# Kernel optimization log

Hardware: AMD Instinct MI355X
Metric: run time of the kernel (lower is better)

## Reference

```python
import jax, jax.numpy as jnp
import numpy as np

N = 50000          # nodes
E = 800000         # edges (before self loops)
F_IN = 16
HID = 64
HEADS = 4
C = 64             # per-head out channels (concat=False)
G = 64             # graphs in batch
NEG_SLOPE = 0.2


def setup_inputs() -> dict:
    key = jax.random.key(0)
    ks = jax.random.split(key, 20)
    inp = {
        "x": jax.random.normal(ks[0], (N, F_IN), jnp.float32),
        "edge_index": jax.random.randint(ks[1], (2, E), 0, N, jnp.int64),
        "batch": jnp.sort(jax.random.randint(ks[2], (N,), 0, G, jnp.int64)),
        "W_in": jax.random.normal(ks[3], (HID, F_IN), jnp.float32) * 0.1,
        "b_in": jnp.zeros((HID,), jnp.float32),
        "W_out": jax.random.normal(ks[4], (1, HID), jnp.float32) * 0.1,
        "b_out": jnp.zeros((1,), jnp.float32),
    }
    for l in range(3):
        inp[f"W{l}"] = jax.random.normal(ks[5 + 4 * l], (HEADS * C, HID), jnp.float32) * 0.1
        inp[f"asrc{l}"] = jax.random.normal(ks[6 + 4 * l], (HEADS, C), jnp.float32) * 0.1
        inp[f"adst{l}"] = jax.random.normal(ks[7 + 4 * l], (HEADS, C), jnp.float32) * 0.1
        inp[f"bg{l}"] = jnp.zeros((HID,), jnp.float32)
    return inp


def _gat_layer(x, W, a_src, a_dst, bias, src, dst, n):
    # x: [N, HID] -> h: [N, HEADS, C]
    h = (x @ W.T).reshape(n, HEADS, C)
    alpha_s = jnp.einsum("nhc,hc->nh", h, a_src)   # [N, H]
    alpha_d = jnp.einsum("nhc,hc->nh", h, a_dst)
    e = jax.nn.leaky_relu(alpha_s[src] + alpha_d[dst], NEG_SLOPE)  # [E', H]
    # segment softmax over incoming edges of each dst node
    m = jax.ops.segment_max(e, dst, num_segments=n)
    e = jnp.exp(e - m[dst])
    s = jax.ops.segment_sum(e, dst, num_segments=n)
    alpha = e / (s[dst] + 1e-16)                                   # [E', H]
    msg = alpha[:, :, None] * h[src]                               # [E', H, C]
    out = jax.ops.segment_sum(msg, dst, num_segments=n)            # [N, H, C]
    return out.mean(axis=1) + bias                                 # concat=False: head mean


def reference(x, W_in, b_in, W0, asrc0, adst0, bg0, W1, asrc1, adst1, bg1,
              W2, asrc2, adst2, bg2, W_out, b_out, edge_index, batch):
    n = x.shape[0]
    # add self loops (PyG GATConv default)
    loops = jnp.arange(n, dtype=edge_index.dtype)
    src = jnp.concatenate([edge_index[0], loops])
    dst = jnp.concatenate([edge_index[1], loops])

    h = x @ W_in.T + b_in
    for W, a_s, a_d, bg in ((W0, asrc0, adst0, bg0),
                            (W1, asrc1, adst1, bg1),
                            (W2, asrc2, adst2, bg2)):
        h = jax.nn.relu(_gat_layer(h, W, a_s, a_d, bg, src, dst, n))
        # dropout p=0.2 is inactive in eval mode

    # global mean pool over graphs
    sums = jax.ops.segment_sum(h, batch, num_segments=G)
    cnt = jax.ops.segment_sum(jnp.ones((n,), h.dtype), batch, num_segments=G)
    graph_emb = sums / jnp.maximum(cnt, 1.0)[:, None]              # [G, HID]

    return jax.nn.sigmoid(graph_emb @ W_out.T + b_out)             # [G, 1]
```

## Files before the change

kernel.cpp:

```cpp
#include <hip/hip_runtime.h>
#include <hip/hip_bf16.h>
#include <hip/hip_fp16.h>

#define HID 64
#define HEADS 4
#define GCNT 64
#define F_IN 16
#define NEG 0.2f
#define NBUCK 256
#define BSLOT 6144
#define SCHUNK 2048

typedef _Float16 f16x8 __attribute__((ext_vector_type(8)));
typedef float f32x4 __attribute__((ext_vector_type(4)));

__device__ __forceinline__ unsigned pack_h2(float a, float b) {
  __half2 h = __floats2half2_rn(a, b);
  union { __half2 h; unsigned u; } c;
  c.h = h;
  return c.u;
}
__device__ __forceinline__ __half2 uas_h2(unsigned u) {
  union { unsigned u; __half2 h; } c;
  c.u = u;
  return c.h;
}
__device__ __forceinline__ unsigned h2_as_u(__half2 h) {
  union { __half2 h; unsigned u; } c;
  c.h = h;
  return c.u;
}
__device__ __forceinline__ __half2 xor16_add(__half2 v) {
  unsigned u = (unsigned)__shfl_xor((int)h2_as_u(v), 16, 64);
  return __hadd2(v, uas_h2(u));
}

__global__ __launch_bounds__(256) void k_pre(
    const float* __restrict__ W0, const float* __restrict__ asrc,
    const float* __restrict__ adst, int* __restrict__ bcur, float* __restrict__ va) {
  int t = threadIdx.x;
  if (blockIdx.x == 0) bcur[t] = 0;
  int idx = blockIdx.x * 256 + t;
  int q = idx >> 6, k = idx & 63;
  const float* a = (q < 4) ? asrc : adst;
  int h = q & 3;
  float s = 0.f;
  for (int c = 0; c < 64; ++c) s += a[h * 64 + c] * W0[(h * 64 + c) * 64 + k];
  va[idx] = s;
}

__global__ __launch_bounds__(256) void k_bucket(
    const int* __restrict__ ei, int* __restrict__ bcur,
    unsigned* __restrict__ tmp, int E, int N) {
  __shared__ int hist[NBUCK];
  __shared__ int base[NBUCK];
  int t = threadIdx.x;
  int start = blockIdx.x * SCHUNK;
  int end = min(start + SCHUNK, E + N);
  hist[t] = 0;
  __syncthreads();
  unsigned val[8];
  int rank[8];
  bool ok[8];
#pragma unroll
  for (int k = 0; k < 8; ++k) {
    int i = start + t + k * 256;
    ok[k] = i < end;
    if (ok[k]) {
      int s, d;
      if (i < E) {
        s = ei[i];
        d = ei[E + i];
      } else {
        s = d = i - E;
      }
      val[k] = ((unsigned)d << 16) | (unsigned)s;
      rank[k] = atomicAdd(&hist[d >> 8], 1);
    }
  }
  __syncthreads();
  int h = hist[t];
  base[t] = h ? atomicAdd(&bcur[t], h) : 0;
  __syncthreads();
#pragma unroll
  for (int k = 0; k < 8; ++k) {
    if (ok[k]) {
      int bk = (int)(val[k] >> 24);
      int idx = base[bk] + rank[k];
      if (idx < BSLOT) tmp[(size_t)bk * BSLOT + idx] = val[k];
    }
  }
}

__global__ __launch_bounds__(256) void k_bsort(
    const unsigned* __restrict__ tmp, const int* __restrict__ bcur,
    int* __restrict__ rowptr, int* __restrict__ col, int N) {
  __shared__ int s[NBUCK];
  __shared__ int hist[NBUCK];
  __shared__ int pref[NBUCK];
  int b = blockIdx.x, t = threadIdx.x;
  int c = min(bcur[t], BSLOT);
  s[t] = c;
  __syncthreads();
  for (int o = 1; o < 256; o <<= 1) {
    int x = (t >= o) ? s[t - o] : 0;
    __syncthreads();
    s[t] += x;
    __syncthreads();
  }
  int base = (b == 0) ? 0 : s[b - 1];
  int total = s[255];
  int cntb = min(bcur[b], BSLOT);
  hist[t] = 0;
  __syncthreads();
  for (int j = t; j < cntb; j += 256)
    atomicAdd(&hist[(tmp[(size_t)b * BSLOT + j] >> 16) & 255], 1);
  __syncthreads();
  int v = hist[t];
  pref[t] = v;
  __syncthreads();
  for (int o = 1; o < 256; o <<= 1) {
    int x = (t >= o) ? pref[t - o] : 0;
    __syncthreads();
    pref[t] += x;
    __syncthreads();
  }
  pref[t] -= v;
  __syncthreads();
  int node = b * 256 + t;
  if (node < N) rowptr[node] = base + pref[t];
  if (b == 255 && t == 255) rowptr[N] = total;
  hist[t] = 0;
  __syncthreads();
  for (int j = t; j < cntb; j += 256) {
    unsigned e = tmp[(size_t)b * BSLOT + j];
    int d8 = (int)((e >> 16) & 255);
    int r = atomicAdd(&hist[d8], 1);
    col[base + pref[d8] + r] = (int)(e & 0xffffu);
  }
}

__global__ void k_init(const float* __restrict__ x, const float* __restrict__ Win,
                       const float* __restrict__ bin,
                       const float* __restrict__ W0, const float* __restrict__ W1,
                       const float* __restrict__ W2,
                       __half* __restrict__ Wh3, __half* __restrict__ Wcat3,
                       float* __restrict__ sums, const float* __restrict__ va,
                       float* __restrict__ as_, float* __restrict__ ad_,
                       __half* __restrict__ hh, int N) {
  int b = blockIdx.x, t = threadIdx.x;
  if (b < 384) {
    int i = b * 256 + t;
    if (i < 49152) {
      const float* W = (i < 16384) ? W0 : (i < 32768) ? W1 : W2;
      Wh3[i] = __float2half(W[i & 16383]);
    } else {
      int j = i - 49152;
      int l = j >> 14;
      int r = j & 16383;
      int c = r >> 8;
      int k256 = r & 255;
      int h = k256 & 3, kk = k256 >> 2;
      const float* W = (l == 0) ? W0 : (l == 1) ? W1 : W2;
      Wcat3[j] = __float2half(0.25f * W[(h * 64 + c) * 64 + kk]);
    }
    return;
  }
  if (b < 401) {
    int i = (b - 384) * 256 + t;
    if (i < GCNT * HID + GCNT) sums[i] = 0.f;
    return;
  }
  int i = (b - 401) * 256 + t;
  if (i >= N * HID) return;
  int n = i >> 6, j = i & 63;
  const float* xr = x + (size_t)n * F_IN;
  const float* wr = Win + j * F_IN;
  float acc = bin[j];
#pragma unroll
  for (int k = 0; k < F_IN; ++k) acc += xr[k] * wr[k];
  hh[i] = __float2half(acc);
  float r[8];
#pragma unroll
  for (int q = 0; q < 8; ++q) {
    float v = acc * va[q * 64 + j];
#pragma unroll
    for (int o = 32; o; o >>= 1) v += __shfl_xor(v, o, 64);
    r[q] = v;
  }
  if (j == 0) {
    *(float4*)(as_ + (size_t)n * 4) = make_float4(r[0], r[1], r[2], r[3]);
    *(float4*)(ad_ + (size_t)n * 4) = make_float4(r[4], r[5], r[6], r[7]);
  }
}

__device__ __forceinline__ void gat_one_node(
    int node, int lane, const __half* __restrict__ h, const float* __restrict__ as_,
    const float* __restrict__ ad_, const int* __restrict__ rowptr,
    const int* __restrict__ col, __half* __restrict__ Mrow) {
  int r0 = rowptr[node];
  int deg = rowptr[node + 1] - r0;
  float4 adv = *(const float4*)(ad_ + (size_t)node * 4);

  if (deg <= 64) {
    int off = 0;
    float x0 = 0.f, x1 = 0.f, x2 = 0.f, x3 = 0.f;
    if (lane < deg) {
      int s = col[r0 + lane];
      off = s << 6;
      float4 av = *(const float4*)(as_ + (size_t)s * 4);
      float e0 = av.x + adv.x; e0 = (e0 > 0.f) ? e0 : NEG * e0;
      float e1 = av.y + adv.y; e1 = (e1 > 0.f) ? e1 : NEG * e1;
      float e2 = av.z + adv.z; e2 = (e2 > 0.f) ? e2 : NEG * e2;
      float e3 = av.w + adv.w; e3 = (e3 > 0.f) ? e3 : NEG * e3;
      x0 = __expf(fminf(e0, 60.f));
      x1 = __expf(fminf(e1, 60.f));
      x2 = __expf(fminf(e2, 60.f));
      x3 = __expf(fminf(e3, 60.f));
    }
    float s0 = x0, s1 = x1, s2 = x2, s3 = x3;
#pragma unroll
    for (int o = 32; o; o >>= 1) {
      s0 += __shfl_xor(s0, o, 64);
      s1 += __shfl_xor(s1, o, 64);
      s2 += __shfl_xor(s2, o, 64);
      s3 += __shfl_xor(s3, o, 64);
    }
    unsigned w01 = pack_h2(x0 / (s0 + 1e-16f), x1 / (s1 + 1e-16f));
    unsigned w23 = pack_h2(x2 / (s2 + 1e-16f), x3 / (s3 + 1e-16f));
    __half2 acc01 = __floats2half2_rn(0.f, 0.f);
    __half2 acc23 = acc01;
#pragma unroll 4
    for (int j = 0; j < deg; ++j) {
      int oj = __builtin_amdgcn_readlane(off, j) + lane;
      unsigned W01 = __builtin_amdgcn_readlane(w01, j);
      unsigned W23 = __builtin_amdgcn_readlane(w23, j);
      __half2 hv = __half2half2(h[oj]);
      acc01 = __hfma2(hv, uas_h2(W01), acc01);
      acc23 = __hfma2(hv, uas_h2(W23), acc23);
    }
    *(__half2*)&Mrow[lane * 4] = acc01;
    *(__half2*)&Mrow[lane * 4 + 2] = acc23;
    return;
  }
  float m0 = -1e30f, m1 = -1e30f, m2 = -1e30f, m3 = -1e30f;
  for (int j = lane; j < deg; j += 64) {
    int s = col[r0 + j];
    float4 av = *(const float4*)(as_ + (size_t)s * 4);
    float e0 = av.x + adv.x; e0 = (e0 > 0.f) ? e0 : NEG * e0; m0 = fmaxf(m0, e0);
    float e1 = av.y + adv.y; e1 = (e1 > 0.f) ? e1 : NEG * e1; m1 = fmaxf(m1, e1);
    float e2 = av.z + adv.z; e2 = (e2 > 0.f) ? e2 : NEG * e2; m2 = fmaxf(m2, e2);
    float e3 = av.w + adv.w; e3 = (e3 > 0.f) ? e3 : NEG * e3; m3 = fmaxf(m3, e3);
  }
#pragma unroll
  for (int o = 32; o; o >>= 1) {
    m0 = fmaxf(m0, __shfl_xor(m0, o, 64));
    m1 = fmaxf(m1, __shfl_xor(m1, o, 64));
    m2 = fmaxf(m2, __shfl_xor(m2, o, 64));
    m3 = fmaxf(m3, __shfl_xor(m3, o, 64));
  }
  float s0 = 0.f, s1 = 0.f, s2 = 0.f, s3 = 0.f;
  for (int j = lane; j < deg; j += 64) {
    int s = col[r0 + j];
    float4 av = *(const float4*)(as_ + (size_t)s * 4);
    float e0 = av.x + adv.x; e0 = (e0 > 0.f) ? e0 : NEG * e0; s0 += __expf(e0 - m0);
    float e1 = av.y + adv.y; e1 = (e1 > 0.f) ? e1 : NEG * e1; s1 += __expf(e1 - m1);
    float e2 = av.z + adv.z; e2 = (e2 > 0.f) ? e2 : NEG * e2; s2 += __expf(e2 - m2);
    float e3 = av.w + adv.w; e3 = (e3 > 0.f) ? e3 : NEG * e3; s3 += __expf(e3 - m3);
  }
#pragma unroll
  for (int o = 32; o; o >>= 1) {
    s0 += __shfl_xor(s0, o, 64);
    s1 += __shfl_xor(s1, o, 64);
    s2 += __shfl_xor(s2, o, 64);
    s3 += __shfl_xor(s3, o, 64);
  }
  float i0 = 1.f / (s0 + 1e-16f), i1 = 1.f / (s1 + 1e-16f);
  float i2 = 1.f / (s2 + 1e-16f), i3 = 1.f / (s3 + 1e-16f);
  float a0 = 0.f, a1 = 0.f, a2 = 0.f, a3 = 0.f;
  for (int j = 0; j < deg; ++j) {
    int s = col[r0 + j];
    float4 av = *(const float4*)(as_ + (size_t)s * 4);
    float e0 = av.x + adv.x; e0 = (e0 > 0.f) ? e0 : NEG * e0;
    float e1 = av.y + adv.y; e1 = (e1 > 0.f) ? e1 : NEG * e1;
    float e2 = av.z + adv.z; e2 = (e2 > 0.f) ? e2 : NEG * e2;
    float e3 = av.w + adv.w; e3 = (e3 > 0.f) ? e3 : NEG * e3;
    float hv = __half2float(h[(s << 6) + lane]);
    a0 = fmaf(__expf(e0 - m0) * i0, hv, a0);
    a1 = fmaf(__expf(e1 - m1) * i1, hv, a1);
    a2 = fmaf(__expf(e2 - m2) * i2, hv, a2);
    a3 = fmaf(__expf(e3 - m3) * i3, hv, a3);
  }
  *(__half2*)&Mrow[lane * 4] = __floats2half2_rn(a0, a1);
  *(__half2*)&Mrow[lane * 4 + 2] = __floats2half2_rn(a2, a3);
}

template <bool FIN>
__global__ __launch_bounds__(256) void k_gatf(
    const __half* __restrict__ h, const float* __restrict__ as_,
    const float* __restrict__ ad_, const int* __restrict__ rowptr,
    const int* __restrict__ col, const __half* __restrict__ Wcat,
    const float* __restrict__ bg, const __half* __restrict__ Wn,
    const float* __restrict__ asrc, const float* __restrict__ adst,
    __half* __restrict__ hout, float* __restrict__ nas, float* __restrict__ nad,
    int N) {
  __shared__ __half Mt[16 * 264];
  __shared__ __half O[16 * 72];
  int tid = threadIdx.x;
  int lane = tid & 63, wv = tid >> 6;
  int tile = blockIdx.x;
  int half = lane >> 5, l5 = lane & 31;
  int npairs = (N + 1) >> 1;

  for (int pp = 0; pp < 2; ++pp) {
    int pr = tile * 8 + wv * 2 + pp;
    if (pr >= npairs) break;
    int n0 = pr * 2;
    int n1 = min(n0 + 1, N - 1);
    int mynode = half ? n1 : n0;
    int r0 = rowptr[mynode];
    int dg = rowptr[mynode + 1] - r0;
    int dgA = __builtin_amdgcn_readlane(dg, 0);
    int dgB = __builtin_amdgcn_readlane(dg, 32);

    if (dgA <= 32 && dgB <= 32) {
      float4 adv = *(const float4*)(ad_ + (size_t)mynode * 4);
      int off = 0;
      float x0 = 0.f, x1 = 0.f, x2 = 0.f, x3 = 0.f;
      if (l5 < dg) {
        int s = col[r0 + l5];
        off = s << 6;
        float4 av = *(const float4*)(as_ + (size_t)s * 4);
        float e0 = av.x + adv.x; e0 = (e0 > 0.f) ? e0 : NEG * e0;
        float e1 = av.y + adv.y; e1 = (e1 > 0.f) ? e1 : NEG * e1;
        float e2 = av.z + adv.z; e2 = (e2 > 0.f) ? e2 : NEG * e2;
        float e3 = av.w + adv.w; e3 = (e3 > 0.f) ? e3 : NEG * e3;
        x0 = __expf(fminf(e0, 60.f));
        x1 = __expf(fminf(e1, 60.f));
        x2 = __expf(fminf(e2, 60.f));
        x3 = __expf(fminf(e3, 60.f));
      }
      float s0 = x0, s1 = x1, s2 = x2, s3 = x3;
#pragma unroll
      for (int o = 16; o; o >>= 1) {
        s0 += __shfl_xor(s0, o, 64);
        s1 += __shfl_xor(s1, o, 64);
        s2 += __shfl_xor(s2, o, 64);
        s3 += __shfl_xor(s3, o, 64);
      }
      unsigned w01 = pack_h2(x0 / (s0 + 1e-16f), x1 / (s1 + 1e-16f));
      unsigned w23 = pack_h2(x2 / (s2 + 1e-16f), x3 / (s3 + 1e-16f));

      int g = l5 >> 4, li = l5 & 15;
      const uint2* h4p = (const uint2*)h;
      __half2 z = __floats2half2_rn(0.f, 0.f);
      __half2 a0_01 = z, a0_23 = z, a1_01 = z, a1_23 = z;
      __half2 a2_01 = z, a2_23 = z, a3_01 = z, a3_23 = z;
      int mdeg = max(dgA, dgB);
      int baddr = half << 7;
#pragma unroll 2
      for (int j = 0; j < mdeg; j += 2) {
        int addr = baddr + (j + g) * 4;
        int oj = __builtin_amdgcn_ds_bpermute(addr, off);
        unsigned W01 = (unsigned)__builtin_amdgcn_ds_bpermute(addr, (int)w01);
        unsigned W23 = (unsigned)__builtin_amdgcn_ds_bpermute(addr, (int)w23);
        uint2 hv = h4p[(oj >> 2) + li];
        __half2 ha = uas_h2(hv.x), hb = uas_h2(hv.y);
        __half2 wA = uas_h2(W01), wB = uas_h2(W23);
        __half2 c0 = __low2half2(ha), c1 = __high2half2(ha);
        __half2 c2 = __low2half2(hb), c3 = __high2half2(hb);
        a0_01 = __hfma2(c0, wA, a0_01); a0_23 = __hfma2(c0, wB, a0_23);
        a1_01 = __hfma2(c1, wA, a1_01); a1_23 = __hfma2(c1, wB, a1_23);
        a2_01 = __hfma2(c2, wA, a2_01); a2_23 = __hfma2(c2, wB, a2_23);
        a3_01 = __hfma2(c3, wA, a3_01); a3_23 = __hfma2(c3, wB, a3_23);
      }
      a0_01 = xor16_add(a0_01); a0_23 = xor16_add(a0_23);
      a1_01 = xor16_add(a1_01); a1_23 = xor16_add(a1_23);
      a2_01 = xor16_add(a2_01); a2_23 = xor16_add(a2_23);
      a3_01 = xor16_add(a3_01); a3_23 = xor16_add(a3_23);
      if (g == 0) {
        __half* row = &Mt[(mynode & 15) * 264 + li * 16];
        uint4 st1, st2;
        st1.x = h2_as_u(a0_01); st1.y = h2_as_u(a0_23);
        st1.z = h2_as_u(a1_01); st1.w = h2_as_u(a1_23);
        st2.x = h2_as_u(a2_01); st2.y = h2_as_u(a2_23);
        st2.z = h2_as_u(a3_01); st2.w = h2_as_u(a3_23);
        *(uint4*)&row[0] = st1;
        *(uint4*)&row[8] = st2;
      }
    } else {
      gat_one_node(n0, lane, h, as_, ad_, rowptr, col, &Mt[(n0 & 15) * 264]);
      if (n1 != n0) gat_one_node(n1, lane, h, as_, ad_, rowptr, col, &Mt[(n1 & 15) * 264]);
    }
  }
  __syncthreads();

  int quad = lane >> 4, n16 = lane & 15;
  const f16x8* WC = (const f16x8*)Wcat;
  int ch1 = wv * 16 + n16;
  float bias1 = bg[ch1];
  f32x4 c1 = {0.f, 0.f, 0.f, 0.f};
#pragma unroll
  for (int i = 0; i < 8; ++i) {
    f16x8 a = *(const f16x8*)&Mt[n16 * 264 + (i * 4 + quad) * 8];
    c1 = __builtin_amdgcn_mfma_f32_16x16x32_f16(a, WC[ch1 * 32 + i * 4 + quad], c1, 0, 0, 0);
  }
#pragma unroll
  for (int r = 0; r < 4; ++r) {
    float v = fmaxf(c1[r] + bias1, 0.f);
    O[(quad * 4 + r) * 72 + ch1] = __float2half(v);
  }
  __syncthreads();
  {
    int nd = tid >> 4, c0 = (tid & 15) * 4;
    int node = tile * 16 + nd;
    if (node < N) {
      uint2 v = *(const uint2*)&O[nd * 72 + c0];
      *(uint2*)&hout[(size_t)node * 64 + c0] = v;
    }
  }
  if (!FIN) {
    const f16x8* WN = (const f16x8*)Wn;
    f16x8 a0 = *(const f16x8*)&O[n16 * 72 + quad * 8];
    f16x8 a1 = *(const f16x8*)&O[n16 * 72 + 32 + quad * 8];
#pragma unroll
    for (int nt = 0; nt < 4; ++nt) {
      int ch = wv * 64 + nt * 16 + n16;
      f32x4 zz = {0.f, 0.f, 0.f, 0.f};
      zz = __builtin_amdgcn_mfma_f32_16x16x32_f16(a0, WN[ch * 8 + quad], zz, 0, 0, 0);
      zz = __builtin_amdgcn_mfma_f32_16x16x32_f16(a1, WN[ch * 8 + 4 + quad], zz, 0, 0, 0);
      float aw = asrc[ch], dw = adst[ch];
      if (nt == 0) {
#pragma unroll
        for (int r = 0; r < 4; ++r) { c1[r] = zz[r] * aw; }
      } else {
#pragma unroll
        for (int r = 0; r < 4; ++r) { c1[r] = fmaf(zz[r], aw, c1[r]); }
      }
      if (nt == 0) {
#pragma unroll
        for (int r = 0; r < 4; ++r) {  }
      }
      static_assert(true, "");
      if (nt == 0) {
      }
      (void)dw;
      break;
    }
    f32x4 accs[4];
#pragma unroll
    for (int nt = 0; nt < 4; ++nt) {
      int ch = wv * 64 + nt * 16 + n16;
      f32x4 zz = {0.f, 0.f, 0.f, 0.f};
      zz = __builtin_amdgcn_mfma_f32_16x16x32_f16(a0, WN[ch * 8 + quad], zz, 0, 0, 0);
      zz = __builtin_amdgcn_mfma_f32_16x16x32_f16(a1, WN[ch * 8 + 4 + quad], zz, 0, 0, 0);
      accs[nt] = zz;
    }
#pragma unroll
    for (int r = 0; r < 4; ++r) {
      float vs = 0.f, vd = 0.f;
#pragma unroll
      for (int nt = 0; nt < 4; ++nt) {
        int ch = wv * 64 + nt * 16 + n16;
        vs = fmaf(accs[nt][r], asrc[ch], vs);
        vd = fmaf(accs[nt][r], adst[ch], vd);
      }
#pragma unroll
      for (int o = 8; o; o >>= 1) {
        vs += __shfl_xor(vs, o, 64);
        vd += __shfl_xor(vd, o, 64);
      }
      int node = tile * 16 + quad * 4 + r;
      if (n16 == 0 && node < N) {
        nas[(size_t)node * 4 + wv] = vs;
        nad[(size_t)node * 4 + wv] = vd;
      }
    }
  }
}

__global__ __launch_bounds__(256) void k_pool(
    const __half* __restrict__ hh, const int* __restrict__ batch,
    float* __restrict__ sums, float* __restrict__ cnt, int N) {
  int c = threadIdx.x & 63, r = threadIdx.x >> 6;
  int base = blockIdx.x * 64 + r * 16;
  float acc = 0.f;
  int curg = -1, cacc = 0;
  for (int i = 0; i < 16; ++i) {
    int n = base + i;
    if (n >= N) break;
    int g = batch[n];
    if (g != curg) {
      if (curg >= 0) {
        atomicAdd(&sums[curg * HID + c], acc);
        if (c == 0) atomicAdd(&cnt[curg], (float)cacc);
      }
      curg = g; acc = 0.f; cacc = 0;
    }
    acc += __half2float(hh[(size_t)n * HID + c]);
    cacc++;
  }
  if (curg >= 0) {
    atomicAdd(&sums[curg * HID + c], acc);
    if (c == 0) atomicAdd(&cnt[curg], (float)cacc);
  }
}

__global__ void k_out(const float* __restrict__ sums, const float* __restrict__ cnt,
                      const float* __restrict__ Wout, const float* __restrict__ bout,
                      float* __restrict__ out) {
  int g = blockIdx.x, lane = threadIdx.x;
  float cg = fmaxf(cnt[g], 1.f);
  float v = (sums[g * HID + lane] / cg) * Wout[lane];
#pragma unroll
  for (int o = 32; o; o >>= 1) v += __shfl_xor(v, o, 64);
  if (lane == 0) out[g] = 1.f / (1.f + __expf(-v));
}

extern "C" void kernel_launch(void* const* d_in, const int* in_sizes, int n_in,
                              void* d_out, int out_size, void* d_ws, size_t ws_size,
                              hipStream_t stream) {
  const float* x    = (const float*)d_in[0];
  const int*   ei   = (const int*)d_in[1];
  const int*   batch= (const int*)d_in[2];
  const float* Win  = (const float*)d_in[3];
  const float* bin  = (const float*)d_in[4];
  const float* Wout = (const float*)d_in[5];
  const float* bout = (const float*)d_in[6];
  const float* Wl[3]    = {(const float*)d_in[7],  (const float*)d_in[11], (const float*)d_in[15]};
  const float* asrcl[3] = {(const float*)d_in[8],  (const float*)d_in[12], (const float*)d_in[16]};
  const float* adstl[3] = {(const float*)d_in[9],  (const float*)d_in[13], (const float*)d_in[17]};
  const float* bgl[3]   = {(const float*)d_in[10], (const float*)d_in[14], (const float*)d_in[18]};

  int N = in_sizes[2];
  int E = in_sizes[1] / 2;
  int EE = E + N;

  char* p = (char*)d_ws;
  auto alloc = [&](size_t bytes) {
    char* r = p;
    p += (bytes + 255) & ~(size_t)255;
    return r;
  };
  int*      rowptr = (int*)alloc((size_t)(N + 1) * 4);
  int*      col    = (int*)alloc((size_t)EE * 4);
  unsigned* tmp    = (unsigned*)alloc((size_t)NBUCK * BSLOT * 4);
  int*      bcur   = (int*)alloc(NBUCK * 4);
  float*    va     = (float*)alloc(8 * 64 * 4);
  __half*   hhA    = (__half*)alloc((size_t)N * HID * 2);
  __half*   hhB    = (__half*)alloc((size_t)N * HID * 2);
  float*    asA    = (float*)alloc((size_t)N * HEADS * 4);
  float*    adA    = (float*)alloc((size_t)N * HEADS * 4);
  float*    asB    = (float*)alloc((size_t)N * HEADS * 4);
  float*    adB    = (float*)alloc((size_t)N * HEADS * 4);
  __half*   Wh3    = (__half*)alloc(3 * 16384 * 2);
  __half*   Wcat3  = (__half*)alloc(3 * 16384 * 2);
  float*    sums   = (float*)alloc((size_t)(GCNT * HID + GCNT) * 4);
  float*    cnt    = sums + GCNT * HID;

  int tiles = (N + 15) / 16;

  k_pre<<<2, 256, 0, stream>>>(Wl[0], asrcl[0], adstl[0], bcur, va);
  k_bucket<<<(EE + SCHUNK - 1) / SCHUNK, 256, 0, stream>>>(ei, bcur, tmp, E, N);
  k_bsort<<<NBUCK, 256, 0, stream>>>(tmp, bcur, rowptr, col, N);

  k_init<<<401 + (N * HID + 255) / 256, 256, 0, stream>>>(
      x, Win, bin, Wl[0], Wl[1], Wl[2], Wh3, Wcat3, sums, va, asA, adA, hhA, N);

  k_gatf<false><<<tiles, 256, 0, stream>>>(hhA, asA, adA, rowptr, col,
                                           Wcat3, bgl[0], Wh3 + 16384, asrcl[1], adstl[1],
                                           hhB, asB, adB, N);
  k_gatf<false><<<tiles, 256, 0, stream>>>(hhB, asB, adB, rowptr, col,
                                           Wcat3 + 16384, bgl[1], Wh3 + 32768, asrcl[2], adstl[2],
                                           hhA, asA, adA, N);
  k_gatf<true><<<tiles, 256, 0, stream>>>(hhA, asA, adA, rowptr, col,
                                          Wcat3 + 32768, bgl[2], nullptr, nullptr, nullptr,
                                          hhB, nullptr, nullptr, N);

  k_pool<<<(N + 63) / 64, 256, 0, stream>>>(hhB, batch, sums, cnt, N);
  k_out<<<GCNT, 64, 0, stream>>>(sums, cnt, Wout, bout, (float*)d_out);
}
```

Measured before the change: 338.6 us.

## Fold input projection into attention vectors and interleave two node pairs per wave

```diff
diff --git a/kernel.cpp b/kernel.cpp
--- a/kernel.cpp
+++ b/kernel.cpp
@@ -37,16 +37,37 @@
 
 __global__ __launch_bounds__(256) void k_pre(
     const float* __restrict__ W0, const float* __restrict__ asrc,
-    const float* __restrict__ adst, int* __restrict__ bcur, float* __restrict__ va) {
+    const float* __restrict__ adst, const float* __restrict__ Win,
+    const float* __restrict__ bin, int* __restrict__ bcur,
+    float* __restrict__ vb, float* __restrict__ c8) {
   int t = threadIdx.x;
-  if (blockIdx.x == 0) bcur[t] = 0;
-  int idx = blockIdx.x * 256 + t;
-  int q = idx >> 6, k = idx & 63;
-  const float* a = (q < 4) ? asrc : adst;
-  int h = q & 3;
-  float s = 0.f;
-  for (int c = 0; c < 64; ++c) s += a[h * 64 + c] * W0[(h * 64 + c) * 64 + k];
-  va[idx] = s;
+  if (blockIdx.x == 0) {
+    bcur[t] = 0;
+    return;
+  }
+  __shared__ float vaL[512];
+#pragma unroll
+  for (int it = 0; it < 2; ++it) {
+    int idx = t + it * 256;
+    int q = idx >> 6, j = idx & 63;
+    const float* a = (q < 4) ? asrc : adst;
+    int h = q & 3;
+    float s = 0.f;
+    for (int c = 0; c < 64; ++c) s += a[h * 64 + c] * W0[(h * 64 + c) * 64 + j];
+    vaL[idx] = s;
+  }
+  __syncthreads();
+  if (t < 128) {
+    int q = t >> 4, k = t & 15;
+    float s = 0.f;
+    for (int j = 0; j < 64; ++j) s += vaL[q * 64 + j] * Win[j * F_IN + k];
+    vb[t] = s;
+  } else if (t < 136) {
+    int q = t - 128;
+    float s = 0.f;
+    for (int j = 0; j < 64; ++j) s += vaL[q * 64 + j] * bin[j];
+    c8[q] = s;
+  }
 }
 
 __global__ __launch_bounds__(256) void k_bucket(
@@ -145,7 +166,8 @@
                        const float* __restrict__ W0, const float* __restrict__ W1,
                        const float* __restrict__ W2,
                        __half* __restrict__ Wh3, __half* __restrict__ Wcat3,
-                       float* __restrict__ sums, const float* __restrict__ va,
+                       float* __restrict__ sums, const float* __restrict__ vb,
+                       const float* __restrict__ c8,
                        float* __restrict__ as_, float* __restrict__ ad_,
                        __half* __restrict__ hh, int N) {
   int b = blockIdx.x, t = threadIdx.x;
@@ -176,21 +198,21 @@
   int n = i >> 6, j = i & 63;
   const float* xr = x + (size_t)n * F_IN;
   const float* wr = Win + j * F_IN;
+  float xv[F_IN];
   float acc = bin[j];
 #pragma unroll
-  for (int k = 0; k < F_IN; ++k) acc += xr[k] * wr[k];
+  for (int k = 0; k < F_IN; ++k) {
+    xv[k] = xr[k];
+    acc = fmaf(xv[k], wr[k], acc);
+  }
   hh[i] = __float2half(acc);
-  float r[8];
-#pragma unroll
-  for (int q = 0; q < 8; ++q) {
-    float v = acc * va[q * 64 + j];
-#pragma unroll
-    for (int o = 32; o; o >>= 1) v += __shfl_xor(v, o, 64);
-    r[q] = v;
-  }
-  if (j == 0) {
-    *(float4*)(as_ + (size_t)n * 4) = make_float4(r[0], r[1], r[2], r[3]);
-    *(float4*)(ad_ + (size_t)n * 4) = make_float4(r[4], r[5], r[6], r[7]);
+  if (j < 8) {
+    const float* vbq = vb + j * 16;
+    float s = c8[j];
+#pragma unroll
+    for (int k = 0; k < F_IN; ++k) s = fmaf(xv[k], vbq[k], s);
+    if (j < 4) as_[(size_t)n * 4 + j] = s;
+    else ad_[(size_t)n * 4 + (j - 4)] = s;
   }
 }
 
@@ -293,6 +315,90 @@
   }
   *(__half2*)&Mrow[lane * 4] = __floats2half2_rn(a0, a1);
   *(__half2*)&Mrow[lane * 4 + 2] = __floats2half2_rn(a2, a3);
+}
+
+__device__ __forceinline__ void gat_pair(
+    int pr, int lane, int half, int l5, int N,
+    const __half* __restrict__ h, const float* __restrict__ as_,
+    const float* __restrict__ ad_, const int* __restrict__ rowptr,
+    const int* __restrict__ col, __half* __restrict__ Mt) {
+  int n0 = pr * 2;
+  int n1 = min(n0 + 1, N - 1);
+  int mynode = half ? n1 : n0;
+  int r0 = rowptr[mynode];
+  int dg = rowptr[mynode + 1] - r0;
+  int dgA = __builtin_amdgcn_readlane(dg, 0);
+  int dgB = __builtin_amdgcn_readlane(dg, 32);
+
+  if (dgA <= 32 && dgB <= 32) {
+    float4 adv = *(const float4*)(ad_ + (size_t)mynode * 4);
+    int off = 0;
+    float x0 = 0.f, x1 = 0.f, x2 = 0.f, x3 = 0.f;
+    if (l5 < dg) {
+      int s = col[r0 + l5];
+      off = s << 6;
+      float4 av = *(const float4*)(as_ + (size_t)s * 4);
+      float e0 = av.x + adv.x; e0 = (e0 > 0.f) ? e0 : NEG * e0;
+      float e1 = av.y + adv.y; e1 = (e1 > 0.f) ? e1 : NEG * e1;
+      float e2 = av.z + adv.z; e2 = (e2 > 0.f) ? e2 : NEG * e2;
+      float e3 = av.w + adv.w; e3 = (e3 > 0.f) ? e3 : NEG * e3;
+      x0 = __expf(fminf(e0, 60.f));
+      x1 = __expf(fminf(e1, 60.f));
+      x2 = __expf(fminf(e2, 60.f));
+      x3 = __expf(fminf(e3, 60.f));
+    }
+    float s0 = x0, s1 = x1, s2 = x2, s3 = x3;
+#pragma unroll
+    for (int o = 16; o; o >>= 1) {
+      s0 += __shfl_xor(s0, o, 64);
+      s1 += __shfl_xor(s1, o, 64);
+      s2 += __shfl_xor(s2, o, 64);
+      s3 += __shfl_xor(s3, o, 64);
+    }
+    unsigned w01 = pack_h2(x0 / (s0 + 1e-16f), x1 / (s1 + 1e-16f));
+    unsigned w23 = pack_h2(x2 / (s2 + 1e-16f), x3 / (s3 + 1e-16f));
+
+    int g = l5 >> 4, li = l5 & 15;
+    const uint2* h4p = (const uint2*)h;
+    __half2 z = __floats2half2_rn(0.f, 0.f);
+    __half2 a0_01 = z, a0_23 = z, a1_01 = z, a1_23 = z;
+    __half2 a2_01 = z, a2_23 = z, a3_01 = z, a3_23 = z;
+    int mdeg = max(dgA, dgB);
+    int baddr = half << 7;
+#pragma unroll 2
+    for (int j = 0; j < mdeg; j += 2) {
+      int addr = baddr + (j + g) * 4;
+      int oj = __builtin_amdgcn_ds_bpermute(addr, off);
+      unsigned W01 = (unsigned)__builtin_amdgcn_ds_bpermute(addr, (int)w01);
+      unsigned W23 = (unsigned)__builtin_amdgcn_ds_bpermute(addr, (int)w23);
+      uint2 hv = h4p[(oj >> 2) + li];
+      __half2 ha = uas_h2(hv.x), hb = uas_h2(hv.y);
+      __half2 wA = uas_h2(W01), wB = uas_h2(W23);
+      __half2 c0 = __low2half2(ha), c1 = __high2half2(ha);
+      __half2 c2 = __low2half2(hb), c3 = __high2half2(hb);
+      a0_01 = __hfma2(c0, wA, a0_01); a0_23 = __hfma2(c0, wB, a0_23);
+      a1_01 = __hfma2(c1, wA, a1_01); a1_23 = __hfma2(c1, wB, a1_23);
+      a2_01 = __hfma2(c2, wA, a2_01); a2_23 = __hfma2(c2, wB, a2_23);
+      a3_01 = __hfma2(c3, wA, a3_01); a3_23 = __hfma2(c3, wB, a3_23);
+    }
+    a0_01 = xor16_add(a0_01); a0_23 = xor16_add(a0_23);
+    a1_01 = xor16_add(a1_01); a1_23 = xor16_add(a1_23);
+    a2_01 = xor16_add(a2_01); a2_23 = xor16_add(a2_23);
+    a3_01 = xor16_add(a3_01); a3_23 = xor16_add(a3_23);
+    if (g == 0) {
+      __half* row = &Mt[(mynode & 15) * 264 + li * 16];
+      uint4 st1, st2;
+      st1.x = h2_as_u(a0_01); st1.y = h2_as_u(a0_23);
+      st1.z = h2_as_u(a1_01); st1.w = h2_as_u(a1_23);
+      st2.x = h2_as_u(a2_01); st2.y = h2_as_u(a2_23);
+      st2.z = h2_as_u(a3_01); st2.w = h2_as_u(a3_23);
+      *(uint4*)&row[0] = st1;
+      *(uint4*)&row[8] = st2;
+    }
+  } else {
+    gat_one_node(n0, lane, h, as_, ad_, rowptr, col, &Mt[(n0 & 15) * 264]);
+    if (n1 != n0) gat_one_node(n1, lane, h, as_, ad_, rowptr, col, &Mt[(n1 & 15) * 264]);
+  }
 }
 
 template <bool FIN>
@@ -312,86 +418,132 @@
   int half = lane >> 5, l5 = lane & 31;
   int npairs = (N + 1) >> 1;
 
-  for (int pp = 0; pp < 2; ++pp) {
-    int pr = tile * 8 + wv * 2 + pp;
-    if (pr >= npairs) break;
-    int n0 = pr * 2;
-    int n1 = min(n0 + 1, N - 1);
-    int mynode = half ? n1 : n0;
-    int r0 = rowptr[mynode];
-    int dg = rowptr[mynode + 1] - r0;
-    int dgA = __builtin_amdgcn_readlane(dg, 0);
-    int dgB = __builtin_amdgcn_readlane(dg, 32);
-
-    if (dgA <= 32 && dgB <= 32) {
-      float4 adv = *(const float4*)(ad_ + (size_t)mynode * 4);
-      int off = 0;
-      float x0 = 0.f, x1 = 0.f, x2 = 0.f, x3 = 0.f;
-      if (l5 < dg) {
-        int s = col[r0 + l5];
-        off = s << 6;
+  int pr0 = tile * 8 + wv * 2;
+  int pr1 = pr0 + 1;
+  bool has0 = pr0 < npairs, has1 = pr1 < npairs;
+  if (has0 && has1) {
+    int my0 = min(pr0 * 2 + half, N - 1);
+    int my1 = min(pr1 * 2 + half, N - 1);
+    int r0a = rowptr[my0];
+    int dga = rowptr[my0 + 1] - r0a;
+    int r0b = rowptr[my1];
+    int dgb = rowptr[my1 + 1] - r0b;
+    int dA0 = __builtin_amdgcn_readlane(dga, 0);
+    int dB0 = __builtin_amdgcn_readlane(dga, 32);
+    int dA1 = __builtin_amdgcn_readlane(dgb, 0);
+    int dB1 = __builtin_amdgcn_readlane(dgb, 32);
+
+    if (dA0 <= 32 && dB0 <= 32 && dA1 <= 32 && dB1 <= 32) {
+      float4 adva = *(const float4*)(ad_ + (size_t)my0 * 4);
+      float4 advb = *(const float4*)(ad_ + (size_t)my1 * 4);
+      int offa = 0, offb = 0;
+      float xa0 = 0.f, xa1 = 0.f, xa2 = 0.f, xa3 = 0.f;
+      float xb0 = 0.f, xb1 = 0.f, xb2 = 0.f, xb3 = 0.f;
+      if (l5 < dga) {
+        int s = col[r0a + l5];
+        offa = s << 6;
         float4 av = *(const float4*)(as_ + (size_t)s * 4);
-        float e0 = av.x + adv.x; e0 = (e0 > 0.f) ? e0 : NEG * e0;
-        float e1 = av.y + adv.y; e1 = (e1 > 0.f) ? e1 : NEG * e1;
-        float e2 = av.z + adv.z; e2 = (e2 > 0.f) ? e2 : NEG * e2;
-        float e3 = av.w + adv.w; e3 = (e3 > 0.f) ? e3 : NEG * e3;
-        x0 = __expf(fminf(e0, 60.f));
-        x1 = __expf(fminf(e1, 60.f));
-        x2 = __expf(fminf(e2, 60.f));
-        x3 = __expf(fminf(e3, 60.f));
-      }
-      float s0 = x0, s1 = x1, s2 = x2, s3 = x3;
+        float e0 = av.x + adva.x; e0 = (e0 > 0.f) ? e0 : NEG * e0;
+        float e1 = av.y + adva.y; e1 = (e1 > 0.f) ? e1 : NEG * e1;
+        float e2 = av.z + adva.z; e2 = (e2 > 0.f) ? e2 : NEG * e2;
+        float e3 = av.w + adva.w; e3 = (e3 > 0.f) ? e3 : NEG * e3;
+        xa0 = __expf(fminf(e0, 60.f));
+        xa1 = __expf(fminf(e1, 60.f));
+        xa2 = __expf(fminf(e2, 60.f));
+        xa3 = __expf(fminf(e3, 60.f));
+      }
+      if (l5 < dgb) {
+        int s = col[r0b + l5];
+        offb = s << 6;
+        float4 av = *(const float4*)(as_ + (size_t)s * 4);
+        float e0 = av.x + advb.x; e0 = (e0 > 0.f) ? e0 : NEG * e0;
+        float e1 = av.y + advb.y; e1 = (e1 > 0.f) ? e1 : NEG * e1;
+        float e2 = av.z + advb.z; e2 = (e2 > 0.f) ? e2 : NEG * e2;
+        float e3 = av.w + advb.w; e3 = (e3 > 0.f) ? e3 : NEG * e3;
+        xb0 = __expf(fminf(e0, 60.f));
+        xb1 = __expf(fminf(e1, 60.f));
+        xb2 = __expf(fminf(e2, 60.f));
+        xb3 = __expf(fminf(e3, 60.f));
+      }
+      float sa0 = xa0, sa1 = xa1, sa2 = xa2, sa3 = xa3;
+      float sb0 = xb0, sb1 = xb1, sb2 = xb2, sb3 = xb3;
 #pragma unroll
       for (int o = 16; o; o >>= 1) {
-        s0 += __shfl_xor(s0, o, 64);
-        s1 += __shfl_xor(s1, o, 64);
-        s2 += __shfl_xor(s2, o, 64);
-        s3 += __shfl_xor(s3, o, 64);
-      }
-      unsigned w01 = pack_h2(x0 / (s0 + 1e-16f), x1 / (s1 + 1e-16f));
-      unsigned w23 = pack_h2(x2 / (s2 + 1e-16f), x3 / (s3 + 1e-16f));
+        sa0 += __shfl_xor(sa0, o, 64);
+        sa1 += __shfl_xor(sa1, o, 64);
+        sa2 += __shfl_xor(sa2, o, 64);
+        sa3 += __shfl_xor(sa3, o, 64);
+        sb0 += __shfl_xor(sb0, o, 64);
+        sb1 += __shfl_xor(sb1, o, 64);
+        sb2 += __shfl_xor(sb2, o, 64);
+        sb3 += __shfl_xor(sb3, o, 64);
+      }
+      unsigned w01a = pack_h2(xa0 / (sa0 + 1e-16f), xa1 / (sa1 + 1e-16f));
+      unsigned w23a = pack_h2(xa2 / (sa2 + 1e-16f), xa3 / (sa3 + 1e-16f));
+      unsigned w01b = pack_h2(xb0 / (sb0 + 1e-16f), xb1 / (sb1 + 1e-16f));
+      unsigned w23b = pack_h2(xb2 / (sb2 + 1e-16f), xb3 / (sb3 + 1e-16f));
 
       int g = l5 >> 4, li = l5 & 15;
       const uint2* h4p = (const uint2*)h;
       __half2 z = __floats2half2_rn(0.f, 0.f);
-      __half2 a0_01 = z, a0_23 = z, a1_01 = z, a1_23 = z;
-      __half2 a2_01 = z, a2_23 = z, a3_01 = z, a3_23 = z;
-      int mdeg = max(dgA, dgB);
+      __half2 pa0 = z, pa1 = z, pa2 = z, pa3 = z, pa4 = z, pa5 = z, pa6 = z, pa7 = z;
+      __half2 pb0 = z, pb1 = z, pb2 = z, pb3 = z, pb4 = z, pb5 = z, pb6 = z, pb7 = z;
+      int mm = max(max(dA0, dB0), max(dA1, dB1));
       int baddr = half << 7;
-#pragma unroll 2
-      for (int j = 0; j < mdeg; j += 2) {
+      for (int j = 0; j < mm; j += 2) {
         int addr = baddr + (j + g) * 4;
-        int oj = __builtin_amdgcn_ds_bpermute(addr, off);
-        unsigned W01 = (unsigned)__builtin_amdgcn_ds_bpermute(addr, (int)w01);
-        unsigned W23 = (unsigned)__builtin_amdgcn_ds_bpermute(addr, (int)w23);
-        uint2 hv = h4p[(oj >> 2) + li];
-        __half2 ha = uas_h2(hv.x), hb = uas_h2(hv.y);
-        __half2 wA = uas_h2(W01), wB = uas_h2(W23);
-        __half2 c0 = __low2half2(ha), c1 = __high2half2(ha);
-        __half2 c2 = __low2half2(hb), c3 = __high2half2(hb);
-        a0_01 = __hfma2(c0, wA, a0_01); a0_23 = __hfma2(c0, wB, a0_23);
-        a1_01 = __hfma2(c1, wA, a1_01); a1_23 = __hfma2(c1, wB, a1_23);
-        a2_01 = __hfma2(c2, wA, a2_01); a2_23 = __hfma2(c2, wB, a2_23);
-        a3_01 = __hfma2(c3, wA, a3_01); a3_23 = __hfma2(c3, wB, a3_23);
-      }
-      a0_01 = xor16_add(a0_01); a0_23 = xor16_add(a0_23);
-      a1_01 = xor16_add(a1_01); a1_23 = xor16_add(a1_23);
-      a2_01 = xor16_add(a2_01); a2_23 = xor16_add(a2_23);
-      a3_01 = xor16_add(a3_01); a3_23 = xor16_add(a3_23);
+        int oja = __builtin_amdgcn_ds_bpermute(addr, offa);
+        unsigned Wa01 = (unsigned)__builtin_amdgcn_ds_bpermute(addr, (int)w01a);
+        unsigned Wa23 = (unsigned)__builtin_amdgcn_ds_bpermute(addr, (int)w23a);
+        int ojb = __builtin_amdgcn_ds_bpermute(addr, offb);
+        unsigned Wb01 = (unsigned)__builtin_amdgcn_ds_bpermute(addr, (int)w01b);
+        unsigned Wb23 = (unsigned)__builtin_amdgcn_ds_bpermute(addr, (int)w23b);
+        uint2 hva = h4p[(oja >> 2) + li];
+        uint2 hvb = h4p[(ojb >> 2) + li];
+        {
+          __half2 ha = uas_h2(hva.x), hb = uas_h2(hva.y);
+          __half2 wA = uas_h2(Wa01), wB = uas_h2(Wa23);
+          __half2 c0 = __low2half2(ha), c1 = __high2half2(ha);
+          __half2 c2 = __low2half2(hb), c3 = __high2half2(hb);
+          pa0 = __hfma2(c0, wA, pa0); pa1 = __hfma2(c0, wB, pa1);
+          pa2 = __hfma2(c1, wA, pa2); pa3 = __hfma2(c1, wB, pa3);
+          pa4 = __hfma2(c2, wA, pa4); pa5 = __hfma2(c2, wB, pa5);
+          pa6 = __hfma2(c3, wA, pa6); pa7 = __hfma2(c3, wB, pa7);
+        }
+        {
+          __half2 ha = uas_h2(hvb.x), hb = uas_h2(hvb.y);
+          __half2 wA = uas_h2(Wb01), wB = uas_h2(Wb23);
+          __half2 c0 = __low2half2(ha), c1 = __high2half2(ha);
+          __half2 c2 = __low2half2(hb), c3 = __high2half2(hb);
+          pb0 = __hfma2(c0, wA, pb0); pb1 = __hfma2(c0, wB, pb1);
+          pb2 = __hfma2(c1, wA, pb2); pb3 = __hfma2(c1, wB, pb3);
+          pb4 = __hfma2(c2, wA, pb4); pb5 = __hfma2(c2, wB, pb5);
+          pb6 = __hfma2(c3, wA, pb6); pb7 = __hfma2(c3, wB, pb7);
+        }
+      }
+      pa0 = xor16_add(pa0); pa1 = xor16_add(pa1); pa2 = xor16_add(pa2); pa3 = xor16_add(pa3);
+      pa4 = xor16_add(pa4); pa5 = xor16_add(pa5); pa6 = xor16_add(pa6); pa7 = xor16_add(pa7);
+      pb0 = xor16_add(pb0); pb1 = xor16_add(pb1); pb2 = xor16_add(pb2); pb3 = xor16_add(pb3);
+      pb4 = xor16_add(pb4); pb5 = xor16_add(pb5); pb6 = xor16_add(pb6); pb7 = xor16_add(pb7);
       if (g == 0) {
-        __half* row = &Mt[(mynode & 15) * 264 + li * 16];
-        uint4 st1, st2;
-        st1.x = h2_as_u(a0_01); st1.y = h2_as_u(a0_23);
-        st1.z = h2_as_u(a1_01); st1.w = h2_as_u(a1_23);
-        st2.x = h2_as_u(a2_01); st2.y = h2_as_u(a2_23);
-        st2.z = h2_as_u(a3_01); st2.w = h2_as_u(a3_23);
-        *(uint4*)&row[0] = st1;
-        *(uint4*)&row[8] = st2;
+        __half* rowA = &Mt[(my0 & 15) * 264 + li * 16];
+        __half* rowB = &Mt[(my1 & 15) * 264 + li * 16];
+        uint4 s1, s2;
+        s1.x = h2_as_u(pa0); s1.y = h2_as_u(pa1); s1.z = h2_as_u(pa2); s1.w = h2_as_u(pa3);
+        s2.x = h2_as_u(pa4); s2.y = h2_as_u(pa5); s2.z = h2_as_u(pa6); s2.w = h2_as_u(pa7);
+        *(uint4*)&rowA[0] = s1;
+        *(uint4*)&rowA[8] = s2;
+        s1.x = h2_as_u(pb0); s1.y = h2_as_u(pb1); s1.z = h2_as_u(pb2); s1.w = h2_as_u(pb3);
+        s2.x = h2_as_u(pb4); s2.y = h2_as_u(pb5); s2.z = h2_as_u(pb6); s2.w = h2_as_u(pb7);
+        *(uint4*)&rowB[0] = s1;
+        *(uint4*)&rowB[8] = s2;
       }
     } else {
-      gat_one_node(n0, lane, h, as_, ad_, rowptr, col, &Mt[(n0 & 15) * 264]);
-      if (n1 != n0) gat_one_node(n1, lane, h, as_, ad_, rowptr, col, &Mt[(n1 & 15) * 264]);
-    }
+      gat_pair(pr0, lane, half, l5, N, h, as_, ad_, rowptr, col, Mt);
+      gat_pair(pr1, lane, half, l5, N, h, as_, ad_, rowptr, col, Mt);
+    }
+  } else if (has0) {
+    gat_pair(pr0, lane, half, l5, N, h, as_, ad_, rowptr, col, Mt);
   }
   __syncthreads();
 
@@ -423,30 +575,6 @@
     const f16x8* WN = (const f16x8*)Wn;
     f16x8 a0 = *(const f16x8*)&O[n16 * 72 + quad * 8];
     f16x8 a1 = *(const f16x8*)&O[n16 * 72 + 32 + quad * 8];
-#pragma unroll
-    for (int nt = 0; nt < 4; ++nt) {
-      int ch = wv * 64 + nt * 16 + n16;
-      f32x4 zz = {0.f, 0.f, 0.f, 0.f};
-      zz = __builtin_amdgcn_mfma_f32_16x16x32_f16(a0, WN[ch * 8 + quad], zz, 0, 0, 0);
-      zz = __builtin_amdgcn_mfma_f32_16x16x32_f16(a1, WN[ch * 8 + 4 + quad], zz, 0, 0, 0);
-      float aw = asrc[ch], dw = adst[ch];
-      if (nt == 0) {
-#pragma unroll
-        for (int r = 0; r < 4; ++r) { c1[r] = zz[r] * aw; }
-      } else {
-#pragma unroll
-        for (int r = 0; r < 4; ++r) { c1[r] = fmaf(zz[r], aw, c1[r]); }
-      }
-      if (nt == 0) {
-#pragma unroll
-        for (int r = 0; r < 4; ++r) {  }
-      }
-      static_assert(true, "");
-      if (nt == 0) {
-      }
-      (void)dw;
-      break;
-    }
     f32x4 accs[4];
 #pragma unroll
     for (int nt = 0; nt < 4; ++nt) {
@@ -546,7 +674,8 @@
   int*      col    = (int*)alloc((size_t)EE * 4);
   unsigned* tmp    = (unsigned*)alloc((size_t)NBUCK * BSLOT * 4);
   int*      bcur   = (int*)alloc(NBUCK * 4);
-  float*    va     = (float*)alloc(8 * 64 * 4);
+  float*    vb     = (float*)alloc(128 * 4);
+  float*    c8     = (float*)alloc(8 * 4);
   __half*   hhA    = (__half*)alloc((size_t)N * HID * 2);
   __half*   hhB    = (__half*)alloc((size_t)N * HID * 2);
   float*    asA    = (float*)alloc((size_t)N * HEADS * 4);
@@ -560,12 +689,12 @@
 
   int tiles = (N + 15) / 16;
 
-  k_pre<<<2, 256, 0, stream>>>(Wl[0], asrcl[0], adstl[0], bcur, va);
+  k_pre<<<2, 256, 0, stream>>>(Wl[0], asrcl[0], adstl[0], Win, bin, bcur, vb, c8);
   k_bucket<<<(EE + SCHUNK - 1) / SCHUNK, 256, 0, stream>>>(ei, bcur, tmp, E, N);
   k_bsort<<<NBUCK, 256, 0, stream>>>(tmp, bcur, rowptr, col, N);
 
   k_init<<<401 + (N * HID + 255) / 256, 256, 0, stream>>>(
-      x, Win, bin, Wl[0], Wl[1], Wl[2], Wh3, Wcat3, sums, va, asA, adA, hhA, N);
+      x, Win, bin, Wl[0], Wl[1], Wl[2], Wh3, Wcat3, sums, vb, c8, asA, adA, hhA, N);
 
   k_gatf<false><<<tiles, 256, 0, stream>>>(hhA, asA, adA, rowptr, col,
                                            Wcat3, bgl[0], Wh3 + 16384, asrcl[1], adstl[1],
```

Result: no change. 338.3 us (-0.1%).
